# Kernel optimization log

Hardware: AMD Instinct MI355X
Metric: run time of the kernel (lower is better)

Reference implementation:

```python
import jax, jax.numpy as jnp
import numpy as np

B, S, D = 2, 4096, 1024
EPS = 1e-05


def setup_inputs() -> dict:
    key = jax.random.key(0)
    ks = jax.random.split(key, 7)
    x = jax.random.normal(ks[0], (B, S, D), dtype=jnp.float32)
    gamma = jnp.ones((D,), dtype=jnp.float32)
    wq, wk, wv, wa, wg, wo = (jax.random.normal(k, (D, D), dtype=jnp.float32) for k in ks[1:7])
    return {"x": x, "gamma": gamma, "wq": wq, "wk": wk, "wv": wv, "wa": wa, "wg": wg, "wo": wo}


def _rmsnorm(x, gamma):
    # original uses sum of squares (not mean) with scale = sqrt(dim)
    ss = jnp.sum(jnp.square(x), axis=-1, keepdims=True)
    inv = jax.lax.rsqrt(ss + EPS)
    return inv * x * gamma * (x.shape[-1] ** 0.5)


def _gate_loop_operator(kv, q, a):
    def binop(e_i, e_j):
        a_i, kv_i = e_i
        a_j, kv_j = e_j
        return (a_j * a_i, a_j * kv_i + kv_j)
    _, y = jax.lax.associative_scan(binop, (a, kv), axis=1)
    return q * y


def reference(x, gamma, wq, wk, wv, wa, wg, wo):
    x = _rmsnorm(x, gamma)
    q = x @ wq
    k = x @ wk
    v = x @ wv
    a = jax.nn.sigmoid(x @ wa)
    g = x @ wg
    kv = k * v
    y = _gate_loop_operator(kv, q, a)
    y = y * jax.nn.silu(g)
    return y @ wo
```

## Files before the change

kernel.cpp:

```cpp
#include <hip/hip_runtime.h>
#include <hip/hip_bf16.h>
#include <cstdint>
#include <cstddef>


typedef __bf16 bf16x8 __attribute__((ext_vector_type(8)));
typedef float f32x4 __attribute__((ext_vector_type(4)));

__device__ __forceinline__ void gload_lds16(const void* g, void* l) {
  __builtin_amdgcn_global_load_lds(
      (const __attribute__((address_space(1))) void*)g,
      (__attribute__((address_space(3))) void*)l,
      16, 0, 0);
}

__global__ __launch_bounds__(256) void wconv_k(
    const float* __restrict__ wq, const float* __restrict__ wk,
    const float* __restrict__ wv, const float* __restrict__ wa,
    const float* __restrict__ wg, const float* __restrict__ wo,
    __hip_bfloat16* __restrict__ wcatT, __hip_bfloat16* __restrict__ woT) {
  __shared__ float t[32][33];
  const float* src;
  __hip_bfloat16* dst;
  switch (blockIdx.z) {
    case 0: src = wq; dst = wcatT; break;
    case 1: src = wk; dst = wcatT + (size_t)1024 * 1024; break;
    case 2: src = wv; dst = wcatT + (size_t)2048 * 1024; break;
    case 3: src = wg; dst = wcatT + (size_t)3072 * 1024; break;
    case 4: src = wa; dst = wcatT + (size_t)4096 * 1024; break;
    default: src = wo; dst = woT; break;
  }
  const int n0 = blockIdx.x * 32;
  const int k0 = blockIdx.y * 32;
  const int tx = threadIdx.x, ty = threadIdx.y;
#pragma unroll
  for (int i = 0; i < 32; i += 8)
    t[ty + i][tx] = src[(size_t)(k0 + ty + i) * 1024 + n0 + tx];
  __syncthreads();
#pragma unroll
  for (int i = 0; i < 32; i += 8)
    dst[(size_t)(n0 + ty + i) * 1024 + k0 + tx] = __float2bfloat16(t[tx][ty + i]);
}

__global__ __launch_bounds__(256) void rmsnorm_k(
    const float* __restrict__ x, const float* __restrict__ gamma,
    __hip_bfloat16* __restrict__ xn) {
  const int row = blockIdx.x;
  const int tid = threadIdx.x;
  const float4 xv = ((const float4*)(x + (size_t)row * 1024))[tid];
  float ss = xv.x * xv.x + xv.y * xv.y + xv.z * xv.z + xv.w * xv.w;
#pragma unroll
  for (int off = 32; off >= 1; off >>= 1) ss += __shfl_xor(ss, off, 64);
  __shared__ float wss[4];
  if ((tid & 63) == 0) wss[tid >> 6] = ss;
  __syncthreads();
  const float total = wss[0] + wss[1] + wss[2] + wss[3];
  const float scale = rsqrtf(total + 1e-5f) * 32.0f;
  const float4 gv = ((const float4*)gamma)[tid];
  union { __hip_bfloat16 h[4]; ushort4 u; } ob;
  ob.h[0] = __float2bfloat16(xv.x * gv.x * scale);
  ob.h[1] = __float2bfloat16(xv.y * gv.y * scale);
  ob.h[2] = __float2bfloat16(xv.z * gv.z * scale);
  ob.h[3] = __float2bfloat16(xv.w * gv.w * scale);
  ((ushort4*)(xn + (size_t)row * 1024))[tid] = ob.u;
}

__global__ __launch_bounds__(256) void gemm_bf16(
    const __hip_bfloat16* __restrict__ A, const __hip_bfloat16* __restrict__ Bt,
    int M, int N, int K,
    __hip_bfloat16* __restrict__ outb, int ldb, int nbcols,
    float* __restrict__ outf, int ldf) {
  __shared__ __align__(16) unsigned short As[128 * 32];
  __shared__ __align__(16) unsigned short Bs[128 * 32];
  const int tid = threadIdx.x;
  const int brow = blockIdx.y * 128;
  const int bcol = blockIdx.x * 128;
  const int lane = tid & 63;
  const int w = tid >> 6;
  const int wm = (w >> 1) * 64;
  const int wn = (w & 1) * 64;
  const int l16 = lane & 15;
  const int k8 = lane >> 4;

  const unsigned short* Ag = (const unsigned short*)A;
  const unsigned short* Bg = (const unsigned short*)Bt;

  const int r0 = tid >> 2;
  const int ch = (tid & 3) * 8;

  f32x4 acc[4][4];
#pragma unroll
  for (int i = 0; i < 4; ++i)
#pragma unroll
    for (int j = 0; j < 4; ++j) acc[i][j] = (f32x4){0.f, 0.f, 0.f, 0.f};

  for (int k0 = 0; k0 < K; k0 += 32) {
    __syncthreads();
    gload_lds16(Ag + (size_t)(brow + r0) * K + k0 + ch, &As[r0 * 32 + ch]);
    gload_lds16(Ag + (size_t)(brow + r0 + 64) * K + k0 + ch, &As[(r0 + 64) * 32 + ch]);
    gload_lds16(Bg + (size_t)(bcol + r0) * K + k0 + ch, &Bs[r0 * 32 + ch]);
    gload_lds16(Bg + (size_t)(bcol + r0 + 64) * K + k0 + ch, &Bs[(r0 + 64) * 32 + ch]);
    __syncthreads();

    bf16x8 af[4], bfr[4];
#pragma unroll
    for (int i = 0; i < 4; ++i)
      af[i] = *(const bf16x8*)&As[(wm + i * 16 + l16) * 32 + k8 * 8];
#pragma unroll
    for (int j = 0; j < 4; ++j)
      bfr[j] = *(const bf16x8*)&Bs[(wn + j * 16 + l16) * 32 + k8 * 8];
#pragma unroll
    for (int i = 0; i < 4; ++i)
#pragma unroll
      for (int j = 0; j < 4; ++j)
        acc[i][j] = __builtin_amdgcn_mfma_f32_16x16x32_bf16(af[i], bfr[j], acc[i][j], 0, 0, 0);
  }

  const int mbase = brow + wm + k8 * 4;
  const int nbase = bcol + wn + l16;
#pragma unroll
  for (int i = 0; i < 4; ++i) {
#pragma unroll
    for (int j = 0; j < 4; ++j) {
      const int n = nbase + j * 16;
#pragma unroll
      for (int r = 0; r < 4; ++r) {
        const int m = mbase + i * 16 + r;
        const float v = acc[i][j][r];
        if (n < nbcols) {
          outb[(size_t)m * ldb + n] = __float2bfloat16(v);
        } else {
          outf[(size_t)m * ldf + (n - nbcols)] = v;
        }
      }
    }
  }
}

__global__ __launch_bounds__(256) void scan_pass1(
    const __hip_bfloat16* __restrict__ qkvg, const float* __restrict__ apre,
    float* __restrict__ Asum, float* __restrict__ Ysum) {
  const int bc = blockIdx.x;
  const int d = blockIdx.y * 256 + threadIdx.x;
  const size_t rowbase = (size_t)(bc >> 5) * 4096 + (size_t)(bc & 31) * 128;
  float y = 0.f, Ap = 1.f;
  for (int s = 0; s < 128; ++s) {
    const size_t r = rowbase + s;
    const float kk = __bfloat162float(qkvg[r * 4096 + 1024 + d]);
    const float vv = __bfloat162float(qkvg[r * 4096 + 2048 + d]);
    const float ap = apre[r * 1024 + d];
    const float a = 1.f / (1.f + __expf(-ap));
    y = fmaf(a, y, kk * vv);
    Ap *= a;
  }
  Asum[(size_t)bc * 1024 + d] = Ap;
  Ysum[(size_t)bc * 1024 + d] = y;
}

__global__ __launch_bounds__(256) void scan_pass2(
    const float* __restrict__ Asum, const float* __restrict__ Ysum,
    float* __restrict__ carry) {
  const int idx = blockIdx.x * 256 + threadIdx.x;
  const int b = idx >> 10, d = idx & 1023;
  float y = 0.f;
  for (int c = 0; c < 32; ++c) {
    const size_t o = (size_t)(b * 32 + c) * 1024 + d;
    carry[o] = y;
    y = fmaf(Asum[o], y, Ysum[o]);
  }
}

__global__ __launch_bounds__(256) void scan_pass3(
    const __hip_bfloat16* __restrict__ qkvg, const float* __restrict__ apre,
    const float* __restrict__ carry, __hip_bfloat16* __restrict__ yact) {
  const int bc = blockIdx.x;
  const int d = blockIdx.y * 256 + threadIdx.x;
  const size_t rowbase = (size_t)(bc >> 5) * 4096 + (size_t)(bc & 31) * 128;
  float y = carry[(size_t)bc * 1024 + d];
  for (int s = 0; s < 128; ++s) {
    const size_t r = rowbase + s;
    const float qq = __bfloat162float(qkvg[r * 4096 + d]);
    const float kk = __bfloat162float(qkvg[r * 4096 + 1024 + d]);
    const float vv = __bfloat162float(qkvg[r * 4096 + 2048 + d]);
    const float gg = __bfloat162float(qkvg[r * 4096 + 3072 + d]);
    const float ap = apre[r * 1024 + d];
    const float a = 1.f / (1.f + __expf(-ap));
    y = fmaf(a, y, kk * vv);
    const float sg = 1.f / (1.f + __expf(-gg));
    yact[r * 1024 + d] = __float2bfloat16(qq * y * gg * sg);
  }
}

extern "C" void kernel_launch(void* const* d_in, const int* in_sizes, int n_in,
                              void* d_out, int out_size, void* d_ws, size_t ws_size,
                              hipStream_t stream) {
  const float* x     = (const float*)d_in[0];
  const float* gamma = (const float*)d_in[1];
  const float* wq    = (const float*)d_in[2];
  const float* wk    = (const float*)d_in[3];
  const float* wv    = (const float*)d_in[4];
  const float* wa    = (const float*)d_in[5];
  const float* wg    = (const float*)d_in[6];
  const float* wo    = (const float*)d_in[7];
  float* out = (float*)d_out;

  char* ws = (char*)d_ws;
  __hip_bfloat16* wcatT = (__hip_bfloat16*)(ws);
  __hip_bfloat16* woT   = (__hip_bfloat16*)(ws + 10485760);
  __hip_bfloat16* xn    = (__hip_bfloat16*)(ws + 12582912);
  __hip_bfloat16* qkvg  = (__hip_bfloat16*)(ws + 29360128);
  float*          apre  = (float*)(ws + 96468992);
  __hip_bfloat16* yact  = (__hip_bfloat16*)(ws + 130023424);
  float*          Asum  = (float*)(ws + 146800640);
  float*          Ysum  = (float*)(ws + 147062784);
  float*          carry = (float*)(ws + 147324928);

  wconv_k<<<dim3(32, 32, 6), dim3(32, 8, 1), 0, stream>>>(wq, wk, wv, wa, wg, wo, wcatT, woT);
  rmsnorm_k<<<dim3(8192), dim3(256), 0, stream>>>(x, gamma, xn);
  gemm_bf16<<<dim3(40, 64), dim3(256), 0, stream>>>(
      xn, wcatT, 8192, 5120, 1024, qkvg, 4096, 4096, apre, 1024);
  scan_pass1<<<dim3(64, 4), dim3(256), 0, stream>>>(qkvg, apre, Asum, Ysum);
  scan_pass2<<<dim3(8), dim3(256), 0, stream>>>(Asum, Ysum, carry);
  scan_pass3<<<dim3(64, 4), dim3(256), 0, stream>>>(qkvg, apre, carry, yact);
  gemm_bf16<<<dim3(8, 64), dim3(256), 0, stream>>>(
      yact, woT, 8192, 1024, 1024, (__hip_bfloat16*)nullptr, 0, 0, out, 1024);
}
```

Before: 232.4 us.

## Replace GEMM with 256x256-tile, 4-stage pipelined, swizzled-LDS kernel

```diff
diff --git a/kernel.cpp b/kernel.cpp
--- a/kernel.cpp
+++ b/kernel.cpp
@@ -65,72 +65,122 @@
   ((ushort4*)(xn + (size_t)row * 1024))[tid] = ob.u;
 }
 
-__global__ __launch_bounds__(256) void gemm_bf16(
+__global__ __launch_bounds__(512, 2) void gemm256(
     const __hip_bfloat16* __restrict__ A, const __hip_bfloat16* __restrict__ Bt,
     int M, int N, int K,
     __hip_bfloat16* __restrict__ outb, int ldb, int nbcols,
     float* __restrict__ outf, int ldf) {
-  __shared__ __align__(16) unsigned short As[128 * 32];
-  __shared__ __align__(16) unsigned short Bs[128 * 32];
+  __shared__ __align__(16) unsigned short As[4 * 8192];
+  __shared__ __align__(16) unsigned short Bs[4 * 8192];
+
   const int tid = threadIdx.x;
-  const int brow = blockIdx.y * 128;
-  const int bcol = blockIdx.x * 128;
+  const int nwg = gridDim.x * gridDim.y;
+  const int bid = blockIdx.y * gridDim.x + blockIdx.x;
+  const int swz = (bid & 7) * (nwg >> 3) + (bid >> 3);
+  const int brow = (swz / gridDim.x) * 256;
+  const int bcol = (swz % gridDim.x) * 256;
+
+  const unsigned short* Ag = (const unsigned short*)A + (size_t)brow * K;
+  const unsigned short* Bg = (const unsigned short*)Bt + (size_t)bcol * K;
+
+  const int srow = tid >> 2;
+  const int sch8 = (((tid & 3) ^ ((srow >> 1) & 3)) << 3);
+
+  auto stageA = [&](int sl) {
+    unsigned short* dst = As + ((sl & 3) << 13);
+    const int k0 = sl << 5;
+    gload_lds16(Ag + (size_t)srow * K + k0 + sch8, dst + tid * 8);
+    gload_lds16(Ag + (size_t)(srow + 128) * K + k0 + sch8, dst + 4096 + tid * 8);
+  };
+  auto stageB = [&](int sl) {
+    unsigned short* dst = Bs + ((sl & 3) << 13);
+    const int k0 = sl << 5;
+    gload_lds16(Bg + (size_t)srow * K + k0 + sch8, dst + tid * 8);
+    gload_lds16(Bg + (size_t)(srow + 128) * K + k0 + sch8, dst + 4096 + tid * 8);
+  };
+
   const int lane = tid & 63;
-  const int w = tid >> 6;
-  const int wm = (w >> 1) * 64;
-  const int wn = (w & 1) * 64;
+  const int wid = tid >> 6;
+  const int wr = wid >> 2;
+  const int wc = wid & 3;
   const int l16 = lane & 15;
   const int k8 = lane >> 4;
 
-  const unsigned short* Ag = (const unsigned short*)A;
-  const unsigned short* Bg = (const unsigned short*)Bt;
-
-  const int r0 = tid >> 2;
-  const int ch = (tid & 3) * 8;
-
-  f32x4 acc[4][4];
-#pragma unroll
-  for (int i = 0; i < 4; ++i)
-#pragma unroll
-    for (int j = 0; j < 4; ++j) acc[i][j] = (f32x4){0.f, 0.f, 0.f, 0.f};
-
-  for (int k0 = 0; k0 < K; k0 += 32) {
-    __syncthreads();
-    gload_lds16(Ag + (size_t)(brow + r0) * K + k0 + ch, &As[r0 * 32 + ch]);
-    gload_lds16(Ag + (size_t)(brow + r0 + 64) * K + k0 + ch, &As[(r0 + 64) * 32 + ch]);
-    gload_lds16(Bg + (size_t)(bcol + r0) * K + k0 + ch, &Bs[r0 * 32 + ch]);
-    gload_lds16(Bg + (size_t)(bcol + r0 + 64) * K + k0 + ch, &Bs[(r0 + 64) * 32 + ch]);
-    __syncthreads();
-
-    bf16x8 af[4], bfr[4];
-#pragma unroll
-    for (int i = 0; i < 4; ++i)
-      af[i] = *(const bf16x8*)&As[(wm + i * 16 + l16) * 32 + k8 * 8];
-#pragma unroll
-    for (int j = 0; j < 4; ++j)
-      bfr[j] = *(const bf16x8*)&Bs[(wn + j * 16 + l16) * 32 + k8 * 8];
-#pragma unroll
-    for (int i = 0; i < 4; ++i)
-#pragma unroll
-      for (int j = 0; j < 4; ++j)
-        acc[i][j] = __builtin_amdgcn_mfma_f32_16x16x32_bf16(af[i], bfr[j], acc[i][j], 0, 0, 0);
-  }
-
-  const int mbase = brow + wm + k8 * 4;
-  const int nbase = bcol + wn + l16;
-#pragma unroll
-  for (int i = 0; i < 4; ++i) {
-#pragma unroll
-    for (int j = 0; j < 4; ++j) {
-      const int n = nbase + j * 16;
+  int aoff[8], boff[4];
+#pragma unroll
+  for (int m = 0; m < 8; ++m) {
+    const int r = wr * 128 + m * 16 + l16;
+    aoff[m] = r * 32 + ((k8 ^ ((r >> 1) & 3)) << 3);
+  }
+#pragma unroll
+  for (int n = 0; n < 4; ++n) {
+    const int r = wc * 64 + n * 16 + l16;
+    boff[n] = r * 32 + ((k8 ^ ((r >> 1) & 3)) << 3);
+  }
+
+  f32x4 acc[8][4];
+#pragma unroll
+  for (int m = 0; m < 8; ++m)
+#pragma unroll
+    for (int n = 0; n < 4; ++n) acc[m][n] = (f32x4){0.f, 0.f, 0.f, 0.f};
+
+  const int NS = K >> 5;
+  stageA(0); stageB(0);
+  stageA(1); stageB(1);
+  stageA(2); stageB(2);
+  asm volatile("s_waitcnt vmcnt(8)" ::: "memory");
+  __builtin_amdgcn_s_barrier();
+
+  for (int s = 0; s < NS; ++s) {
+    const unsigned short* As_s = As + ((s & 3) << 13);
+    const unsigned short* Bs_s = Bs + ((s & 3) << 13);
+    bf16x8 af[8], bfr[4];
+#pragma unroll
+    for (int m = 0; m < 8; ++m) af[m] = *(const bf16x8*)(As_s + aoff[m]);
+    bfr[0] = *(const bf16x8*)(Bs_s + boff[0]);
+    bfr[1] = *(const bf16x8*)(Bs_s + boff[1]);
+    if (s + 3 < NS) stageA(s + 3);
+    __builtin_amdgcn_s_barrier();
+    __builtin_amdgcn_s_setprio(1);
+#pragma unroll
+    for (int m = 0; m < 8; ++m) {
+      acc[m][0] = __builtin_amdgcn_mfma_f32_16x16x32_bf16(af[m], bfr[0], acc[m][0], 0, 0, 0);
+      acc[m][1] = __builtin_amdgcn_mfma_f32_16x16x32_bf16(af[m], bfr[1], acc[m][1], 0, 0, 0);
+    }
+    __builtin_amdgcn_s_setprio(0);
+    __builtin_amdgcn_s_barrier();
+    bfr[2] = *(const bf16x8*)(Bs_s + boff[2]);
+    bfr[3] = *(const bf16x8*)(Bs_s + boff[3]);
+    if (s + 3 < NS) stageB(s + 3);
+    __builtin_amdgcn_s_barrier();
+    __builtin_amdgcn_s_setprio(1);
+#pragma unroll
+    for (int m = 0; m < 8; ++m) {
+      acc[m][2] = __builtin_amdgcn_mfma_f32_16x16x32_bf16(af[m], bfr[2], acc[m][2], 0, 0, 0);
+      acc[m][3] = __builtin_amdgcn_mfma_f32_16x16x32_bf16(af[m], bfr[3], acc[m][3], 0, 0, 0);
+    }
+    __builtin_amdgcn_s_setprio(0);
+    if (s < NS - 3)       asm volatile("s_waitcnt vmcnt(8)" ::: "memory");
+    else if (s == NS - 3) asm volatile("s_waitcnt vmcnt(4)" ::: "memory");
+    else if (s == NS - 2) asm volatile("s_waitcnt vmcnt(0)" ::: "memory");
+    __builtin_amdgcn_s_barrier();
+  }
+
+  const int mb = brow + wr * 128 + k8 * 4;
+  const int nb = bcol + wc * 64 + l16;
+#pragma unroll
+  for (int m = 0; m < 8; ++m) {
+#pragma unroll
+    for (int n = 0; n < 4; ++n) {
+      const int col = nb + n * 16;
 #pragma unroll
       for (int r = 0; r < 4; ++r) {
-        const int m = mbase + i * 16 + r;
-        const float v = acc[i][j][r];
-        if (n < nbcols) {
-          outb[(size_t)m * ldb + n] = __float2bfloat16(v);
+        const int row = mb + m * 16 + r;
+        const float v = acc[m][n][r];
+        if (col < nbcols) {
+          outb[(size_t)row * ldb + col] = __float2bfloat16(v);
         } else {
-          outf[(size_t)m * ldf + (n - nbcols)] = v;
+          outf[(size_t)row * ldf + (col - nbcols)] = v;
         }
       }
     }
@@ -217,11 +267,11 @@
 
   wconv_k<<<dim3(32, 32, 6), dim3(32, 8, 1), 0, stream>>>(wq, wk, wv, wa, wg, wo, wcatT, woT);
   rmsnorm_k<<<dim3(8192), dim3(256), 0, stream>>>(x, gamma, xn);
-  gemm_bf16<<<dim3(40, 64), dim3(256), 0, stream>>>(
+  gemm256<<<dim3(20, 32), dim3(512), 0, stream>>>(
       xn, wcatT, 8192, 5120, 1024, qkvg, 4096, 4096, apre, 1024);
   scan_pass1<<<dim3(64, 4), dim3(256), 0, stream>>>(qkvg, apre, Asum, Ysum);
   scan_pass2<<<dim3(8), dim3(256), 0, stream>>>(Asum, Ysum, carry);
   scan_pass3<<<dim3(64, 4), dim3(256), 0, stream>>>(qkvg, apre, carry, yact);
-  gemm_bf16<<<dim3(8, 64), dim3(256), 0, stream>>>(
+  gemm256<<<dim3(4, 32), dim3(512), 0, stream>>>(
       yact, woT, 8192, 1024, 1024, (__hip_bfloat16*)nullptr, 0, 0, out, 1024);
 }
```

After: 220.6 us. 1.05x faster.
